# Kernel tuning notes

Hardware: AMD Instinct MI355X
Metric: run time of the kernel (lower is better)

Reference implementation:

```python
import math
import jax, jax.numpy as jnp
import numpy as np

BSZ, N_HEADS, N_KV_HEADS, SEQLEN, HEAD_DIM = 1, 32, 8, 2048, 128
DIM = N_HEADS * HEAD_DIM  # 4096
N_REP = N_HEADS // N_KV_HEADS  # 4
NEG = -1e9


def setup_inputs() -> dict:
    key = jax.random.key(0)
    kq, kk, kv = jax.random.split(key, 3)
    q = jax.random.normal(kq, (BSZ, N_HEADS, SEQLEN, HEAD_DIM), dtype=jnp.float32)
    k = jax.random.normal(kk, (BSZ, N_KV_HEADS, SEQLEN, HEAD_DIM), dtype=jnp.float32)
    v = jax.random.normal(kv, (BSZ, N_KV_HEADS, SEQLEN, HEAD_DIM), dtype=jnp.float32)
    # additive causal mask: 0 on/below diagonal, large negative above
    causal = jnp.tril(jnp.ones((SEQLEN, SEQLEN), dtype=bool))
    mask = jnp.where(causal, 0.0, NEG).astype(jnp.float32)
    input_pos = jnp.zeros((1,), dtype=jnp.int64)
    return {"input_pos": input_pos, "q": q, "k": k, "v": v,
            "bsz": BSZ, "seqlen": SEQLEN, "mask": mask}


def reference(input_pos, q, k, v, bsz, seqlen, mask):
    # repeat_kv: (b, n_kv, s, d) -> (b, n_kv*n_rep, s, d), repeat_interleave on head dim
    k = jnp.repeat(k, N_REP, axis=1)
    v = jnp.repeat(v, N_REP, axis=1)
    scale = 1.0 / math.sqrt(q.shape[-1])
    # (b, h, s, s)
    attn = jnp.einsum("bhqd,bhkd->bhqk", q, k) * scale + mask
    attn = jax.nn.softmax(attn, axis=-1)
    y = jnp.einsum("bhqk,bhkd->bhqd", attn, v)  # (b, h, s, d)
    return y.transpose(0, 2, 1, 3).reshape(bsz, seqlen, DIM)
```

## Files before the change

### kernel.cpp

```cpp
#include <hip/hip_runtime.h>
#include <hip/hip_bf16.h>

#define SEQ 2048
#define HD 128
#define NH 32
#define NKV 8
#define ODIM 4096
#define QB 64
#define KVB 64
#define SCALE 0.08838834764831845f
#define SCALE_L2E 0.12752767f
#define NEGBIG -1e9f
#define NEGBIG_L2 -1.4426950e9f
#define THR_L2 11.54f

typedef __attribute__((ext_vector_type(8))) short bf16x8;
typedef __attribute__((ext_vector_type(4))) float f32x4;

__device__ __forceinline__ unsigned short f2bf(float x) {
  union { __hip_bfloat16 b; unsigned short u; } c;
  c.b = __float2bfloat16(x);
  return c.u;
}

__device__ __forceinline__ unsigned pack2bf(float lo, float hi) {
  union { __hip_bfloat162 h; unsigned u; } c;
  c.h = __float22bfloat162_rn(float2{lo, hi});
  return c.u;
}

__device__ __forceinline__ void gload_lds16(const unsigned char* g, unsigned char* l) {
  __builtin_amdgcn_global_load_lds(
      (const __attribute__((address_space(1))) void*)g,
      (__attribute__((address_space(3))) void*)l, 16, 0, 0);
}

#define KWORK (NKV * SEQ * 16)
#define VWORK (NKV * (SEQ / 2) * 16)
__global__ __launch_bounds__(256) void sdpa_prepass(
    const float* __restrict__ k, const float* __restrict__ v,
    unsigned char* __restrict__ ws) {
  unsigned char* kimg = ws;
  unsigned char* vimg = ws + (NKV * 32 * 16384);
  int idx = (int)blockIdx.x * 256 + (int)threadIdx.x;
  if (idx < KWORK) {
    int hkv = idx >> 15;
    int rem = idx & 32767;
    int rg = rem >> 4;
    int c8 = (rem & 15) << 3;
    const float* src = k + ((size_t)hkv * SEQ + rg) * HD + c8;
    float4 a = *(const float4*)(src);
    float4 b = *(const float4*)(src + 4);
    union { unsigned short hh[8]; uint4 u4; } pk;
    pk.hh[0]=f2bf(a.x); pk.hh[1]=f2bf(a.y); pk.hh[2]=f2bf(a.z); pk.hh[3]=f2bf(a.w);
    pk.hh[4]=f2bf(b.x); pk.hh[5]=f2bf(b.y); pk.hh[6]=f2bf(b.z); pk.hh[7]=f2bf(b.w);
    int t = rg >> 6, r = rg & 63;
    size_t base = ((size_t)(hkv * 32 + t)) << 14;
    *(uint4*)(kimg + base + (r << 8) + ((c8 << 1) ^ ((r & 7) << 4))) = pk.u4;
  } else {
    int u = idx - KWORK;
    if (u >= VWORK) return;
    int hkv = u >> 14;
    int rem = u & 16383;
    int pr = rem >> 4;
    int d0 = (rem & 15) << 3;
    int rg = pr << 1;
    const float* s0 = v + ((size_t)hkv * SEQ + rg) * HD + d0;
    const float* s1 = s0 + HD;
    float4 a0 = *(const float4*)(s0);
    float4 b0 = *(const float4*)(s0 + 4);
    float4 a1 = *(const float4*)(s1);
    float4 b1 = *(const float4*)(s1 + 4);
    float lo[8] = {a0.x,a0.y,a0.z,a0.w,b0.x,b0.y,b0.z,b0.w};
    float hi[8] = {a1.x,a1.y,a1.z,a1.w,b1.x,b1.y,b1.z,b1.w};
    int t = rg >> 6, rr = rg & 63;
    size_t base = ((size_t)(hkv * 32 + t)) << 14;
    int rb = rr << 1;
    #pragma unroll
    for (int j = 0; j < 8; ++j) {
      int d = d0 + j;
      *(unsigned*)(vimg + base + (d << 7) + (rb ^ ((d & 7) << 4))) =
          pack2bf(lo[j], hi[j]);
    }
  }
}

__global__ __launch_bounds__(512, 4) void sdpa_flash_kernel(
    const float* __restrict__ q, const unsigned char* __restrict__ kimg,
    const unsigned char* __restrict__ vimg, float* __restrict__ out) {
  __shared__ __align__(16) unsigned char smem[65536];
  const int tid = threadIdx.x;
  const int w = tid >> 6;
  const int l = tid & 63;
  const int lm = l & 15;
  const int lg = l >> 4;

  const int p = (int)blockIdx.x;
  const int qtA = p;
  const int qtB = 31 - p;
  const int myqt = (w < 4) ? qtA : qtB;
  const int h = (int)blockIdx.y;
  const int hkv = h >> 2;
  const int qbase = myqt * QB + 16 * (w & 3);
  const int myrow = qbase + lm;

  bf16x8 qa[4];
  {
    const float* qr = q + ((size_t)(h * SEQ + myrow)) * HD + 8 * lg;
    #pragma unroll
    for (int c = 0; c < 4; ++c) {
      float4 a = *(const float4*)(qr + 32 * c);
      float4 b = *(const float4*)(qr + 32 * c + 4);
      union { unsigned short hh[8]; bf16x8 vv; } pk;
      pk.hh[0] = f2bf(a.x * SCALE_L2E); pk.hh[1] = f2bf(a.y * SCALE_L2E);
      pk.hh[2] = f2bf(a.z * SCALE_L2E); pk.hh[3] = f2bf(a.w * SCALE_L2E);
      pk.hh[4] = f2bf(b.x * SCALE_L2E); pk.hh[5] = f2bf(b.y * SCALE_L2E);
      pk.hh[6] = f2bf(b.z * SCALE_L2E); pk.hh[7] = f2bf(b.w * SCALE_L2E);
      qa[c] = pk.vv;
    }
  }

  f32x4 o[8];
  #pragma unroll
  for (int i = 0; i < 8; ++i) o[i] = (f32x4){0.f, 0.f, 0.f, 0.f};
  float mrow = -1e30f;
  float lrow = 0.f;

  const int ntiles = qtB + 1;
  const unsigned char* kt0 = kimg + (((size_t)(hkv * 32)) << 14);
  const unsigned char* vt0 = vimg + (((size_t)(hkv * 32)) << 14);
  const int woff = w << 10;

#define STAGE(tt, bufbase) {                                                 \
    const unsigned char* ks_ = kt0 + (((size_t)(tt)) << 14);                 \
    const unsigned char* vs_ = vt0 + (((size_t)(tt)) << 14);                 \
    unsigned char* Kb_ = (bufbase);                                          \
    unsigned char* Vb_ = (bufbase) + 16384;                                  \
    gload_lds16(ks_ + woff + (l << 4), Kb_ + woff);                          \
    gload_lds16(ks_ + 8192 + woff + (l << 4), Kb_ + 8192 + woff);            \
    gload_lds16(vs_ + woff + (l << 4), Vb_ + woff);                          \
    gload_lds16(vs_ + 8192 + woff + (l << 4), Vb_ + 8192 + woff);            \
  }

  STAGE(0, smem);
  __syncthreads();
  int cur = 0;

  for (int t = 0; t < ntiles; ++t) {
    const int kv0 = t * KVB;
    if (t + 1 < ntiles) STAGE(t + 1, smem + ((cur ^ 1) << 15));

    unsigned char* Klds = smem + (cur << 15);
    unsigned char* Vlds = Klds + 16384;

    if (t <= myqt) {
      f32x4 s[4];
      #pragma unroll
      for (int nt = 0; nt < 4; ++nt) s[nt] = (f32x4){0.f, 0.f, 0.f, 0.f};
      __builtin_amdgcn_s_setprio(1);
      #pragma unroll
      for (int nt = 0; nt < 4; ++nt) {
        int r = (nt << 4) + lm;
        #pragma unroll
        for (int kc = 0; kc < 4; ++kc) {
          int byte = (r << 8) + (((kc << 6) + (lg << 4)) ^ ((r & 7) << 4));
          bf16x8 kb = *(const bf16x8*)(Klds + byte);
          s[nt] = __builtin_amdgcn_mfma_f32_16x16x32_bf16(kb, qa[kc], s[nt], 0, 0, 0);
        }
      }
      __builtin_amdgcn_s_setprio(0);

      if (kv0 + KVB - 1 > qbase) {
        #pragma unroll
        for (int nt = 0; nt < 4; ++nt) {
          #pragma unroll
          for (int i = 0; i < 4; ++i) {
            int col = kv0 + (nt << 4) + (lg << 2) + i;
            s[nt][i] += (col > myrow) ? NEGBIG_L2 : 0.f;
          }
        }
      }

      float tm = -1e30f;
      #pragma unroll
      for (int nt = 0; nt < 4; ++nt)
        #pragma unroll
        for (int i = 0; i < 4; ++i) tm = fmaxf(tm, s[nt][i]);
      tm = fmaxf(tm, __shfl_xor(tm, 16));
      tm = fmaxf(tm, __shfl_xor(tm, 32));
      if (!__all(tm <= mrow + THR_L2)) {
        float mn = fmaxf(mrow, tm);
        float fac = __builtin_amdgcn_exp2f(mrow - mn);
        mrow = mn;
        lrow *= fac;
        #pragma unroll
        for (int nt2 = 0; nt2 < 8; ++nt2) {
          #pragma unroll
          for (int i = 0; i < 4; ++i) o[nt2][i] *= fac;
        }
      }
      float rs = 0.f;
      #pragma unroll
      for (int nt = 0; nt < 4; ++nt) {
        #pragma unroll
        for (int i = 0; i < 4; ++i) {
          float pv = __builtin_amdgcn_exp2f(s[nt][i] - mrow);
          s[nt][i] = pv;
          rs += pv;
        }
      }
      rs += __shfl_xor(rs, 16);
      rs += __shfl_xor(rs, 32);
      lrow += rs;

      unsigned pk0[4], pk1[4];
      #pragma unroll
      for (int nt = 0; nt < 4; ++nt) {
        pk0[nt] = pack2bf(s[nt][0], s[nt][1]);
        pk1[nt] = pack2bf(s[nt][2], s[nt][3]);
      }
      const int srcA = lm + ((lg & 1) << 5);
      const int srcB = srcA + 16;
      const bool lo2 = (lg < 2);
      bf16x8 pb[2];
      #pragma unroll
      for (int kc = 0; kc < 2; ++kc) {
        int a0 = __shfl((int)pk0[2*kc], srcA), b0 = __shfl((int)pk0[2*kc+1], srcA);
        int a1 = __shfl((int)pk1[2*kc], srcA), b1 = __shfl((int)pk1[2*kc+1], srcA);
        int a2 = __shfl((int)pk0[2*kc], srcB), b2 = __shfl((int)pk0[2*kc+1], srcB);
        int a3 = __shfl((int)pk1[2*kc], srcB), b3 = __shfl((int)pk1[2*kc+1], srcB);
        union { int uu[4]; bf16x8 v; } pw;
        pw.uu[0] = lo2 ? a0 : b0;
        pw.uu[1] = lo2 ? a1 : b1;
        pw.uu[2] = lo2 ? a2 : b2;
        pw.uu[3] = lo2 ? a3 : b3;
        pb[kc] = pw.v;
      }

      __builtin_amdgcn_s_setprio(1);
      #pragma unroll
      for (int nt2 = 0; nt2 < 8; ++nt2) {
        int dr = (nt2 << 4) + lm;
        #pragma unroll
        for (int kc = 0; kc < 2; ++kc) {
          int byte = (dr << 7) + (((kc << 6) + (lg << 4)) ^ ((dr & 7) << 4));
          bf16x8 vb = *(const bf16x8*)(Vlds + byte);
          o[nt2] = __builtin_amdgcn_mfma_f32_16x16x32_bf16(vb, pb[kc], o[nt2], 0, 0, 0);
        }
      }
      __builtin_amdgcn_s_setprio(0);
    }

    __syncthreads();
    cur ^= 1;
  }

  float inv = 1.f / lrow;
  float* orow = out + (size_t)myrow * ODIM + h * HD + (lg << 2);
  #pragma unroll
  for (int nt2 = 0; nt2 < 8; ++nt2) {
    float4 st = {o[nt2][0] * inv, o[nt2][1] * inv, o[nt2][2] * inv, o[nt2][3] * inv};
    *(float4*)(orow + (nt2 << 4)) = st;
  }
#undef STAGE
}

__global__ __launch_bounds__(512, 4) void sdpa_flash_fb(
    const float* __restrict__ q, const float* __restrict__ k,
    const float* __restrict__ v, float* __restrict__ out) {
  __shared__ __align__(16) unsigned char smem[65536];
  const int tid = threadIdx.x;
  const int w = tid >> 6;
  const int l = tid & 63;
  const int lm = l & 15;
  const int lg = l >> 4;
  const int p = (int)blockIdx.x;
  const int qtA = p;
  const int qtB = 31 - p;
  const int myqt = (w < 4) ? qtA : qtB;
  const int h = (int)blockIdx.y;
  const int hkv = h >> 2;
  const int qbase = myqt * QB + 16 * (w & 3);
  const int myrow = qbase + lm;
  bf16x8 qa[4];
  {
    const float* qr = q + ((size_t)(h * SEQ + myrow)) * HD + 8 * lg;
    #pragma unroll
    for (int c = 0; c < 4; ++c) {
      float4 a = *(const float4*)(qr + 32 * c);
      float4 b = *(const float4*)(qr + 32 * c + 4);
      union { unsigned short hh[8]; bf16x8 vv; } pk;
      pk.hh[0] = f2bf(a.x * SCALE); pk.hh[1] = f2bf(a.y * SCALE);
      pk.hh[2] = f2bf(a.z * SCALE); pk.hh[3] = f2bf(a.w * SCALE);
      pk.hh[4] = f2bf(b.x * SCALE); pk.hh[5] = f2bf(b.y * SCALE);
      pk.hh[6] = f2bf(b.z * SCALE); pk.hh[7] = f2bf(b.w * SCALE);
      qa[c] = pk.vv;
    }
  }
  f32x4 o[8];
  #pragma unroll
  for (int i = 0; i < 8; ++i) o[i] = (f32x4){0.f, 0.f, 0.f, 0.f};
  float mrow = -1e30f;
  float lrow = 0.f;
  const int ntiles = qtB + 1;
  const float* kg0 = k + (size_t)hkv * SEQ * HD;
  const float* vg0 = v + (size_t)hkv * SEQ * HD;
  const int k_r0 = tid >> 4;
  const int k_c8 = (tid & 15) << 3;
  const int v_rr = (tid & 31) << 1;
  const int v_d0 = (tid >> 5) << 3;
  float4 ka0, kb0, ka1, kb1, va0, vb0, va1, vb1;
#define LOADT(tt) {                                                          \
    const float* kg_ = kg0 + (size_t)((tt) * KVB) * HD + k_r0 * HD + k_c8;   \
    ka0 = *(const float4*)(kg_);                                             \
    kb0 = *(const float4*)(kg_ + 4);                                         \
    ka1 = *(const float4*)(kg_ + 32 * HD);                                   \
    kb1 = *(const float4*)(kg_ + 32 * HD + 4);                               \
    const float* vg_ = vg0 + (size_t)((tt) * KVB) * HD + v_rr * HD + v_d0;   \
    va0 = *(const float4*)(vg_);                                             \
    vb0 = *(const float4*)(vg_ + 4);                                         \
    va1 = *(const float4*)(vg_ + HD);                                        \
    vb1 = *(const float4*)(vg_ + HD + 4);                                    \
  }
#define WRITELDS(bufbase) {                                                  \
    unsigned char* Kb_ = (bufbase);                                          \
    unsigned char* Vb_ = (bufbase) + 16384;                                  \
    {                                                                        \
      union { unsigned short hh[8]; uint4 u4; } pk_;                         \
      pk_.hh[0]=f2bf(ka0.x); pk_.hh[1]=f2bf(ka0.y);                          \
      pk_.hh[2]=f2bf(ka0.z); pk_.hh[3]=f2bf(ka0.w);                          \
      pk_.hh[4]=f2bf(kb0.x); pk_.hh[5]=f2bf(kb0.y);                          \
      pk_.hh[6]=f2bf(kb0.z); pk_.hh[7]=f2bf(kb0.w);                          \
      int byte_ = (k_r0 << 8) + ((k_c8 << 1) ^ ((k_r0 & 7) << 4));           \
      *(uint4*)(Kb_ + byte_) = pk_.u4;                                       \
    }                                                                        \
    {                                                                        \
      int r1_ = k_r0 + 32;                                                   \
      union { unsigned short hh[8]; uint4 u4; } pk_;                         \
      pk_.hh[0]=f2bf(ka1.x); pk_.hh[1]=f2bf(ka1.y);                          \
      pk_.hh[2]=f2bf(ka1.z); pk_.hh[3]=f2bf(ka1.w);                          \
      pk_.hh[4]=f2bf(kb1.x); pk_.hh[5]=f2bf(kb1.y);                          \
      pk_.hh[6]=f2bf(kb1.z); pk_.hh[7]=f2bf(kb1.w);                          \
      int byte_ = (r1_ << 8) + ((k_c8 << 1) ^ ((r1_ & 7) << 4));             \
      *(uint4*)(Kb_ + byte_) = pk_.u4;                                       \
    }                                                                        \
    {                                                                        \
      unsigned w0_ = pack2bf(va0.x, va1.x), w1_ = pack2bf(va0.y, va1.y);     \
      unsigned w2_ = pack2bf(va0.z, va1.z), w3_ = pack2bf(va0.w, va1.w);     \
      unsigned w4_ = pack2bf(vb0.x, vb1.x), w5_ = pack2bf(vb0.y, vb1.y);     \
      unsigned w6_ = pack2bf(vb0.z, vb1.z), w7_ = pack2bf(vb0.w, vb1.w);     \
      int rb_ = v_rr << 1;                                                   \
      int d_;                                                                \
      d_ = v_d0;     *(unsigned*)(Vb_ + (d_ << 7) + (rb_ ^ ((d_ & 7) << 4))) = w0_; \
      d_ = v_d0 + 1; *(unsigned*)(Vb_ + (d_ << 7) + (rb_ ^ ((d_ & 7) << 4))) = w1_; \
      d_ = v_d0 + 2; *(unsigned*)(Vb_ + (d_ << 7) + (rb_ ^ ((d_ & 7) << 4))) = w2_; \
      d_ = v_d0 + 3; *(unsigned*)(Vb_ + (d_ << 7) + (rb_ ^ ((d_ & 7) << 4))) = w3_; \
      d_ = v_d0 + 4; *(unsigned*)(Vb_ + (d_ << 7) + (rb_ ^ ((d_ & 7) << 4))) = w4_; \
      d_ = v_d0 + 5; *(unsigned*)(Vb_ + (d_ << 7) + (rb_ ^ ((d_ & 7) << 4))) = w5_; \
      d_ = v_d0 + 6; *(unsigned*)(Vb_ + (d_ << 7) + (rb_ ^ ((d_ & 7) << 4))) = w6_; \
      d_ = v_d0 + 7; *(unsigned*)(Vb_ + (d_ << 7) + (rb_ ^ ((d_ & 7) << 4))) = w7_; \
    }                                                                        \
  }
  LOADT(0);
  WRITELDS(smem);
  __syncthreads();
  int cur = 0;
  for (int t = 0; t < ntiles; ++t) {
    const int kv0 = t * KVB;
    const bool have_next = (t + 1 < ntiles);
    if (have_next) LOADT(t + 1);
    unsigned char* Klds = smem + (cur << 15);
    unsigned char* Vlds = Klds + 16384;
    if (t <= myqt) {
      f32x4 s[4];
      #pragma unroll
      for (int nt = 0; nt < 4; ++nt) s[nt] = (f32x4){0.f, 0.f, 0.f, 0.f};
      #pragma unroll
      for (int nt = 0; nt < 4; ++nt) {
        int r = (nt << 4) + lm;
        #pragma unroll
        for (int kc = 0; kc < 4; ++kc) {
          int byte = (r << 8) + (((kc << 6) + (lg << 4)) ^ ((r & 7) << 4));
          bf16x8 kb = *(const bf16x8*)(Klds + byte);
          s[nt] = __builtin_amdgcn_mfma_f32_16x16x32_bf16(kb, qa[kc], s[nt], 0, 0, 0);
        }
      }
      if (kv0 + KVB - 1 > qbase) {
        #pragma unroll
        for (int nt = 0; nt < 4; ++nt) {
          #pragma unroll
          for (int i = 0; i < 4; ++i) {
            int col = kv0 + (nt << 4) + (lg << 2) + i;
            s[nt][i] += (col > myrow) ? NEGBIG : 0.f;
          }
        }
      }
      float tm = -1e30f;
      #pragma unroll
      for (int nt = 0; nt < 4; ++nt)
        #pragma unroll
        for (int i = 0; i < 4; ++i) tm = fmaxf(tm, s[nt][i]);
      tm = fmaxf(tm, __shfl_xor(tm, 16));
      tm = fmaxf(tm, __shfl_xor(tm, 32));
      float mn = fmaxf(mrow, tm);
      float fac = __expf(mrow - mn);
      mrow = mn;
      float rs = 0.f;
      #pragma unroll
      for (int nt = 0; nt < 4; ++nt) {
        #pragma unroll
        for (int i = 0; i < 4; ++i) {
          float pv = __expf(s[nt][i] - mn);
          s[nt][i] = pv;
          rs += pv;
        }
      }
      rs += __shfl_xor(rs, 16);
      rs += __shfl_xor(rs, 32);
      lrow = lrow * fac + rs;
      #pragma unroll
      for (int nt2 = 0; nt2 < 8; ++nt2) {
        #pragma unroll
        for (int i = 0; i < 4; ++i) o[nt2][i] *= fac;
      }
      unsigned pk0[4], pk1[4];
      #pragma unroll
      for (int nt = 0; nt < 4; ++nt) {
        pk0[nt] = pack2bf(s[nt][0], s[nt][1]);
        pk1[nt] = pack2bf(s[nt][2], s[nt][3]);
      }
      const int srcA = lm + ((lg & 1) << 5);
      const int srcB = srcA + 16;
      const bool lo2 = (lg < 2);
      bf16x8 pb[2];
      #pragma unroll
      for (int kc = 0; kc < 2; ++kc) {
        int a0 = __shfl((int)pk0[2*kc], srcA), b0 = __shfl((int)pk0[2*kc+1], srcA);
        int a1 = __shfl((int)pk1[2*kc], srcA), b1 = __shfl((int)pk1[2*kc+1], srcA);
        int a2 = __shfl((int)pk0[2*kc], srcB), b2 = __shfl((int)pk0[2*kc+1], srcB);
        int a3 = __shfl((int)pk1[2*kc], srcB), b3 = __shfl((int)pk1[2*kc+1], srcB);
        union { int uu[4]; bf16x8 v; } pw;
        pw.uu[0] = lo2 ? a0 : b0;
        pw.uu[1] = lo2 ? a1 : b1;
        pw.uu[2] = lo2 ? a2 : b2;
        pw.uu[3] = lo2 ? a3 : b3;
        pb[kc] = pw.v;
      }
      #pragma unroll
      for (int nt2 = 0; nt2 < 8; ++nt2) {
        int dr = (nt2 << 4) + lm;
        #pragma unroll
        for (int kc = 0; kc < 2; ++kc) {
          int byte = (dr << 7) + (((kc << 6) + (lg << 4)) ^ ((dr & 7) << 4));
          bf16x8 vb = *(const bf16x8*)(Vlds + byte);
          o[nt2] = __builtin_amdgcn_mfma_f32_16x16x32_bf16(vb, pb[kc], o[nt2], 0, 0, 0);
        }
      }
    }
    if (have_next) {
      WRITELDS(smem + ((cur ^ 1) << 15));
    }
    __syncthreads();
    cur ^= 1;
  }
  float inv = 1.f / lrow;
  float* orow = out + (size_t)myrow * ODIM + h * HD + (lg << 2);
  #pragma unroll
  for (int nt2 = 0; nt2 < 8; ++nt2) {
    float4 st = {o[nt2][0] * inv, o[nt2][1] * inv, o[nt2][2] * inv, o[nt2][3] * inv};
    *(float4*)(orow + (nt2 << 4)) = st;
  }
#undef LOADT
#undef WRITELDS
}

extern "C" void kernel_launch(void* const* d_in, const int* in_sizes, int n_in,
                              void* d_out, int out_size, void* d_ws, size_t ws_size,
                              hipStream_t stream) {
  const float* q = (const float*)d_in[1];
  const float* k = (const float*)d_in[2];
  const float* v = (const float*)d_in[3];
  float* out = (float*)d_out;
  dim3 grid(SEQ / QB / 2, NH);
  const size_t need = (size_t)(NKV * 32 * 16384) * 2;
  if (ws_size >= need && d_ws != nullptr) {
    unsigned char* ws = (unsigned char*)d_ws;
    int total = KWORK + VWORK;
    sdpa_prepass<<<(total + 255) / 256, 256, 0, stream>>>(k, v, ws);
    sdpa_flash_kernel<<<grid, 512, 0, stream>>>(
        q, ws, ws + (NKV * 32 * 16384), out);
  } else {
    sdpa_flash_fb<<<grid, 512, 0, stream>>>(q, k, v, out);
  }
}
```

Measured before the change: 85.98 us.

## Shrink KV tile to 32 rows and use one q-tile per 256-thread block

Halves the KV tile from 64 to 32 rows and re-lays out the prepacked V image to match 32-row tiles. Drops the paired-q-tile scheme: each 256-thread block now handles a single 64-row query tile, launched in descending tile order, with per-wave causal tile limits that skip fully masked half-tiles. The aim is to cut wasted masked compute at the diagonal and let more, smaller blocks share each CU. In exchange it runs twice as many KV-loop iterations, each with a barrier, and load balancing now depends on dispatch order rather than explicit pairing.

```diff
diff --git a/kernel.cpp b/kernel.cpp
--- a/kernel.cpp
+++ b/kernel.cpp
@@ -8,6 +8,7 @@
 #define ODIM 4096
 #define QB 64
 #define KVB 64
+#define KVT 32
 #define SCALE 0.08838834764831845f
 #define SCALE_L2E 0.12752767f
 #define NEGBIG -1e9f
@@ -41,7 +42,7 @@
     const float* __restrict__ k, const float* __restrict__ v,
     unsigned char* __restrict__ ws) {
   unsigned char* kimg = ws;
-  unsigned char* vimg = ws + (NKV * 32 * 16384);
+  unsigned char* vimg = ws + ((size_t)NKV << 19);
   int idx = (int)blockIdx.x * 256 + (int)threadIdx.x;
   if (idx < KWORK) {
     int hkv = idx >> 15;
@@ -54,9 +55,8 @@
     union { unsigned short hh[8]; uint4 u4; } pk;
     pk.hh[0]=f2bf(a.x); pk.hh[1]=f2bf(a.y); pk.hh[2]=f2bf(a.z); pk.hh[3]=f2bf(a.w);
     pk.hh[4]=f2bf(b.x); pk.hh[5]=f2bf(b.y); pk.hh[6]=f2bf(b.z); pk.hh[7]=f2bf(b.w);
-    int t = rg >> 6, r = rg & 63;
-    size_t base = ((size_t)(hkv * 32 + t)) << 14;
-    *(uint4*)(kimg + base + (r << 8) + ((c8 << 1) ^ ((r & 7) << 4))) = pk.u4;
+    size_t base = ((size_t)hkv << 19) + ((size_t)rg << 8);
+    *(uint4*)(kimg + base + ((c8 << 1) ^ ((rg & 7) << 4))) = pk.u4;
   } else {
     int u = idx - KWORK;
     if (u >= VWORK) return;
@@ -73,35 +73,32 @@
     float4 b1 = *(const float4*)(s1 + 4);
     float lo[8] = {a0.x,a0.y,a0.z,a0.w,b0.x,b0.y,b0.z,b0.w};
     float hi[8] = {a1.x,a1.y,a1.z,a1.w,b1.x,b1.y,b1.z,b1.w};
-    int t = rg >> 6, rr = rg & 63;
-    size_t base = ((size_t)(hkv * 32 + t)) << 14;
-    int rb = rr << 1;
+    int t32 = rg >> 5;
+    size_t base = ((size_t)(hkv * 64 + t32)) << 13;
+    int rb = (rg & 31) << 1;
     #pragma unroll
     for (int j = 0; j < 8; ++j) {
       int d = d0 + j;
-      *(unsigned*)(vimg + base + (d << 7) + (rb ^ ((d & 7) << 4))) =
+      *(unsigned*)(vimg + base + (d << 6) + (rb ^ ((d & 3) << 4))) =
           pack2bf(lo[j], hi[j]);
     }
   }
 }
 
-__global__ __launch_bounds__(512, 4) void sdpa_flash_kernel(
+__global__ __launch_bounds__(256, 4) void sdpa_flash_kernel(
     const float* __restrict__ q, const unsigned char* __restrict__ kimg,
     const unsigned char* __restrict__ vimg, float* __restrict__ out) {
-  __shared__ __align__(16) unsigned char smem[65536];
+  __shared__ __align__(16) unsigned char smem[32768];
   const int tid = threadIdx.x;
   const int w = tid >> 6;
   const int l = tid & 63;
   const int lm = l & 15;
   const int lg = l >> 4;
 
-  const int p = (int)blockIdx.x;
-  const int qtA = p;
-  const int qtB = 31 - p;
-  const int myqt = (w < 4) ? qtA : qtB;
+  const int qt = 31 - (int)blockIdx.x;
   const int h = (int)blockIdx.y;
   const int hkv = h >> 2;
-  const int qbase = myqt * QB + 16 * (w & 3);
+  const int qbase = qt * QB + 16 * w;
   const int myrow = qbase + lm;
 
   bf16x8 qa[4];
@@ -126,20 +123,21 @@
   float mrow = -1e30f;
   float lrow = 0.f;
 
-  const int ntiles = qtB + 1;
-  const unsigned char* kt0 = kimg + (((size_t)(hkv * 32)) << 14);
-  const unsigned char* vt0 = vimg + (((size_t)(hkv * 32)) << 14);
-  const int woff = w << 10;
+  const int ntiles = 2 * qt + 2;
+  const int tlim = 2 * qt + (w >> 1);
+  const unsigned char* kt0 = kimg + ((size_t)hkv << 19);
+  const unsigned char* vt0 = vimg + ((size_t)hkv << 19);
+  const int woff = w << 11;
 
 #define STAGE(tt, bufbase) {                                                 \
-    const unsigned char* ks_ = kt0 + (((size_t)(tt)) << 14);                 \
-    const unsigned char* vs_ = vt0 + (((size_t)(tt)) << 14);                 \
+    const unsigned char* ks_ = kt0 + (((size_t)(tt)) << 13);                 \
+    const unsigned char* vs_ = vt0 + (((size_t)(tt)) << 13);                 \
     unsigned char* Kb_ = (bufbase);                                          \
-    unsigned char* Vb_ = (bufbase) + 16384;                                  \
+    unsigned char* Vb_ = (bufbase) + 8192;                                   \
     gload_lds16(ks_ + woff + (l << 4), Kb_ + woff);                          \
-    gload_lds16(ks_ + 8192 + woff + (l << 4), Kb_ + 8192 + woff);            \
+    gload_lds16(ks_ + woff + 1024 + (l << 4), Kb_ + woff + 1024);            \
     gload_lds16(vs_ + woff + (l << 4), Vb_ + woff);                          \
-    gload_lds16(vs_ + 8192 + woff + (l << 4), Vb_ + 8192 + woff);            \
+    gload_lds16(vs_ + woff + 1024 + (l << 4), Vb_ + woff + 1024);            \
   }
 
   STAGE(0, smem);
@@ -147,19 +145,19 @@
   int cur = 0;
 
   for (int t = 0; t < ntiles; ++t) {
-    const int kv0 = t * KVB;
-    if (t + 1 < ntiles) STAGE(t + 1, smem + ((cur ^ 1) << 15));
-
-    unsigned char* Klds = smem + (cur << 15);
-    unsigned char* Vlds = Klds + 16384;
-
-    if (t <= myqt) {
-      f32x4 s[4];
-      #pragma unroll
-      for (int nt = 0; nt < 4; ++nt) s[nt] = (f32x4){0.f, 0.f, 0.f, 0.f};
+    const int kv0 = t * KVT;
+    if (t + 1 < ntiles) STAGE(t + 1, smem + ((cur ^ 1) << 14));
+
+    unsigned char* Klds = smem + (cur << 14);
+    unsigned char* Vlds = Klds + 8192;
+
+    if (t <= tlim) {
+      f32x4 s[2];
+      #pragma unroll
+      for (int nt = 0; nt < 2; ++nt) s[nt] = (f32x4){0.f, 0.f, 0.f, 0.f};
       __builtin_amdgcn_s_setprio(1);
       #pragma unroll
-      for (int nt = 0; nt < 4; ++nt) {
+      for (int nt = 0; nt < 2; ++nt) {
         int r = (nt << 4) + lm;
         #pragma unroll
         for (int kc = 0; kc < 4; ++kc) {
@@ -170,9 +168,9 @@
       }
       __builtin_amdgcn_s_setprio(0);
 
-      if (kv0 + KVB - 1 > qbase) {
-        #pragma unroll
-        for (int nt = 0; nt < 4; ++nt) {
+      if (kv0 + KVT - 1 > qbase) {
+        #pragma unroll
+        for (int nt = 0; nt < 2; ++nt) {
           #pragma unroll
           for (int i = 0; i < 4; ++i) {
             int col = kv0 + (nt << 4) + (lg << 2) + i;
@@ -183,7 +181,7 @@
 
       float tm = -1e30f;
       #pragma unroll
-      for (int nt = 0; nt < 4; ++nt)
+      for (int nt = 0; nt < 2; ++nt)
         #pragma unroll
         for (int i = 0; i < 4; ++i) tm = fmaxf(tm, s[nt][i]);
       tm = fmaxf(tm, __shfl_xor(tm, 16));
@@ -201,7 +199,7 @@
       }
       float rs = 0.f;
       #pragma unroll
-      for (int nt = 0; nt < 4; ++nt) {
+      for (int nt = 0; nt < 2; ++nt) {
         #pragma unroll
         for (int i = 0; i < 4; ++i) {
           float pv = __builtin_amdgcn_exp2f(s[nt][i] - mrow);
@@ -213,40 +211,36 @@
       rs += __shfl_xor(rs, 32);
       lrow += rs;
 
-      unsigned pk0[4], pk1[4];
-      #pragma unroll
-      for (int nt = 0; nt < 4; ++nt) {
+      unsigned pk0[2], pk1[2];
+      #pragma unroll
+      for (int nt = 0; nt < 2; ++nt) {
         pk0[nt] = pack2bf(s[nt][0], s[nt][1]);
         pk1[nt] = pack2bf(s[nt][2], s[nt][3]);
       }
       const int srcA = lm + ((lg & 1) << 5);
       const int srcB = srcA + 16;
       const bool lo2 = (lg < 2);
-      bf16x8 pb[2];
-      #pragma unroll
-      for (int kc = 0; kc < 2; ++kc) {
-        int a0 = __shfl((int)pk0[2*kc], srcA), b0 = __shfl((int)pk0[2*kc+1], srcA);
-        int a1 = __shfl((int)pk1[2*kc], srcA), b1 = __shfl((int)pk1[2*kc+1], srcA);
-        int a2 = __shfl((int)pk0[2*kc], srcB), b2 = __shfl((int)pk0[2*kc+1], srcB);
-        int a3 = __shfl((int)pk1[2*kc], srcB), b3 = __shfl((int)pk1[2*kc+1], srcB);
+      bf16x8 pb;
+      {
+        int a0 = __shfl((int)pk0[0], srcA), b0 = __shfl((int)pk0[1], srcA);
+        int a1 = __shfl((int)pk1[0], srcA), b1 = __shfl((int)pk1[1], srcA);
+        int a2 = __shfl((int)pk0[0], srcB), b2 = __shfl((int)pk0[1], srcB);
+        int a3 = __shfl((int)pk1[0], srcB), b3 = __shfl((int)pk1[1], srcB);
         union { int uu[4]; bf16x8 v; } pw;
         pw.uu[0] = lo2 ? a0 : b0;
         pw.uu[1] = lo2 ? a1 : b1;
         pw.uu[2] = lo2 ? a2 : b2;
         pw.uu[3] = lo2 ? a3 : b3;
-        pb[kc] = pw.v;
+        pb = pw.v;
       }
 
       __builtin_amdgcn_s_setprio(1);
       #pragma unroll
       for (int nt2 = 0; nt2 < 8; ++nt2) {
         int dr = (nt2 << 4) + lm;
-        #pragma unroll
-        for (int kc = 0; kc < 2; ++kc) {
-          int byte = (dr << 7) + (((kc << 6) + (lg << 4)) ^ ((dr & 7) << 4));
-          bf16x8 vb = *(const bf16x8*)(Vlds + byte);
-          o[nt2] = __builtin_amdgcn_mfma_f32_16x16x32_bf16(vb, pb[kc], o[nt2], 0, 0, 0);
-        }
+        int byte = (dr << 6) + ((lg << 4) ^ ((dr & 3) << 4));
+        bf16x8 vb = *(const bf16x8*)(Vlds + byte);
+        o[nt2] = __builtin_amdgcn_mfma_f32_16x16x32_bf16(vb, pb, o[nt2], 0, 0, 0);
       }
       __builtin_amdgcn_s_setprio(0);
     }
@@ -481,15 +475,16 @@
   const float* k = (const float*)d_in[2];
   const float* v = (const float*)d_in[3];
   float* out = (float*)d_out;
-  dim3 grid(SEQ / QB / 2, NH);
-  const size_t need = (size_t)(NKV * 32 * 16384) * 2;
+  const size_t need = ((size_t)NKV << 19) * 2;
   if (ws_size >= need && d_ws != nullptr) {
     unsigned char* ws = (unsigned char*)d_ws;
     int total = KWORK + VWORK;
     sdpa_prepass<<<(total + 255) / 256, 256, 0, stream>>>(k, v, ws);
-    sdpa_flash_kernel<<<grid, 512, 0, stream>>>(
-        q, ws, ws + (NKV * 32 * 16384), out);
+    dim3 grid(SEQ / QB, NH);
+    sdpa_flash_kernel<<<grid, 256, 0, stream>>>(
+        q, ws, ws + ((size_t)NKV << 19), out);
   } else {
-    sdpa_flash_fb<<<grid, 512, 0, stream>>>(q, k, v, out);
-  }
-}
+    dim3 gridf(SEQ / QB / 2, NH);
+    sdpa_flash_fb<<<gridf, 512, 0, stream>>>(q, k, v, out);
+  }
+}
```

New measurement: 137.0 us. +59.4%, slower.

## Software-pipeline QK^T of next tile with softmax and PV of previous tile

Applied to the files above, without the earlier changes.

Restructures the flash-attention loop so each iteration computes QK^T scores for tile t while doing softmax and PV for tile t-1, carrying scores in registers. V moves to a 3-slot LDS ring (LDS grows to 80KB), with K double-buffered separately, and an epilogue drains the last tile. The aim is to overlap MFMA work with the exp/shuffle softmax chain. In exchange it raises register and LDS pressure, which can lower occupancy, and the final-tile handling for waves with smaller myqt relies on subtle slot bookkeeping.

```diff
diff --git a/kernel.cpp b/kernel.cpp
--- a/kernel.cpp
+++ b/kernel.cpp
@@ -88,7 +88,8 @@
 __global__ __launch_bounds__(512, 4) void sdpa_flash_kernel(
     const float* __restrict__ q, const unsigned char* __restrict__ kimg,
     const unsigned char* __restrict__ vimg, float* __restrict__ out) {
-  __shared__ __align__(16) unsigned char smem[65536];
+  __shared__ __align__(16) unsigned char smem[81920];
+  unsigned char* Vring = smem + 32768;
   const int tid = threadIdx.x;
   const int w = tid >> 6;
   const int l = tid & 63;
@@ -131,61 +132,75 @@
   const unsigned char* vt0 = vimg + (((size_t)(hkv * 32)) << 14);
   const int woff = w << 10;
 
-#define STAGE(tt, bufbase) {                                                 \
+#define STAGE(tt, Kb, Vb) {                                                  \
     const unsigned char* ks_ = kt0 + (((size_t)(tt)) << 14);                 \
     const unsigned char* vs_ = vt0 + (((size_t)(tt)) << 14);                 \
-    unsigned char* Kb_ = (bufbase);                                          \
-    unsigned char* Vb_ = (bufbase) + 16384;                                  \
-    gload_lds16(ks_ + woff + (l << 4), Kb_ + woff);                          \
-    gload_lds16(ks_ + 8192 + woff + (l << 4), Kb_ + 8192 + woff);            \
-    gload_lds16(vs_ + woff + (l << 4), Vb_ + woff);                          \
-    gload_lds16(vs_ + 8192 + woff + (l << 4), Vb_ + 8192 + woff);            \
-  }
-
-  STAGE(0, smem);
+    gload_lds16(ks_ + woff + (l << 4), (Kb) + woff);                         \
+    gload_lds16(ks_ + 8192 + woff + (l << 4), (Kb) + 8192 + woff);           \
+    gload_lds16(vs_ + woff + (l << 4), (Vb) + woff);                         \
+    gload_lds16(vs_ + 8192 + woff + (l << 4), (Vb) + 8192 + woff);           \
+  }
+
+  STAGE(0, smem, Vring);
   __syncthreads();
-  int cur = 0;
+
+  f32x4 sp0, sp1, sp2, sp3;
+  int slot_cur = 0;
+  int slot_prev = 0;
 
   for (int t = 0; t < ntiles; ++t) {
     const int kv0 = t * KVB;
-    if (t + 1 < ntiles) STAGE(t + 1, smem + ((cur ^ 1) << 15));
-
-    unsigned char* Klds = smem + (cur << 15);
-    unsigned char* Vlds = Klds + 16384;
-
-    if (t <= myqt) {
-      f32x4 s[4];
-      #pragma unroll
-      for (int nt = 0; nt < 4; ++nt) s[nt] = (f32x4){0.f, 0.f, 0.f, 0.f};
+    int slot_next = slot_cur + 1; if (slot_next == 3) slot_next = 0;
+    if (t + 1 < ntiles)
+      STAGE(t + 1, smem + ((t + 1) & 1) * 16384, Vring + slot_next * 16384);
+
+    unsigned char* Klds = smem + (t & 1) * 16384;
+
+    f32x4 sc0, sc1, sc2, sc3;
+    const bool doQK = (t <= myqt);
+    if (doQK) {
+      sc0 = (f32x4){0.f,0.f,0.f,0.f}; sc1 = (f32x4){0.f,0.f,0.f,0.f};
+      sc2 = (f32x4){0.f,0.f,0.f,0.f}; sc3 = (f32x4){0.f,0.f,0.f,0.f};
       __builtin_amdgcn_s_setprio(1);
       #pragma unroll
-      for (int nt = 0; nt < 4; ++nt) {
-        int r = (nt << 4) + lm;
-        #pragma unroll
-        for (int kc = 0; kc < 4; ++kc) {
-          int byte = (r << 8) + (((kc << 6) + (lg << 4)) ^ ((r & 7) << 4));
-          bf16x8 kb = *(const bf16x8*)(Klds + byte);
-          s[nt] = __builtin_amdgcn_mfma_f32_16x16x32_bf16(kb, qa[kc], s[nt], 0, 0, 0);
+      for (int kc = 0; kc < 4; ++kc) {
+        int r0 = lm;
+        int byte0 = (r0 << 8) + (((kc << 6) + (lg << 4)) ^ ((r0 & 7) << 4));
+        bf16x8 kb0 = *(const bf16x8*)(Klds + byte0);
+        sc0 = __builtin_amdgcn_mfma_f32_16x16x32_bf16(kb0, qa[kc], sc0, 0, 0, 0);
+        int r1 = 16 + lm;
+        int byte1 = (r1 << 8) + (((kc << 6) + (lg << 4)) ^ ((r1 & 7) << 4));
+        bf16x8 kb1 = *(const bf16x8*)(Klds + byte1);
+        sc1 = __builtin_amdgcn_mfma_f32_16x16x32_bf16(kb1, qa[kc], sc1, 0, 0, 0);
+        int r2 = 32 + lm;
+        int byte2 = (r2 << 8) + (((kc << 6) + (lg << 4)) ^ ((r2 & 7) << 4));
+        bf16x8 kb2 = *(const bf16x8*)(Klds + byte2);
+        sc2 = __builtin_amdgcn_mfma_f32_16x16x32_bf16(kb2, qa[kc], sc2, 0, 0, 0);
+        int r3 = 48 + lm;
+        int byte3 = (r3 << 8) + (((kc << 6) + (lg << 4)) ^ ((r3 & 7) << 4));
+        bf16x8 kb3 = *(const bf16x8*)(Klds + byte3);
+        sc3 = __builtin_amdgcn_mfma_f32_16x16x32_bf16(kb3, qa[kc], sc3, 0, 0, 0);
+      }
+      __builtin_amdgcn_s_setprio(0);
+      if (kv0 + KVB - 1 > qbase) {
+        #pragma unroll
+        for (int i = 0; i < 4; ++i) {
+          int colb = kv0 + (lg << 2) + i;
+          sc0[i] += (colb > myrow) ? NEGBIG_L2 : 0.f;
+          sc1[i] += (colb + 16 > myrow) ? NEGBIG_L2 : 0.f;
+          sc2[i] += (colb + 32 > myrow) ? NEGBIG_L2 : 0.f;
+          sc3[i] += (colb + 48 > myrow) ? NEGBIG_L2 : 0.f;
         }
       }
-      __builtin_amdgcn_s_setprio(0);
-
-      if (kv0 + KVB - 1 > qbase) {
-        #pragma unroll
-        for (int nt = 0; nt < 4; ++nt) {
-          #pragma unroll
-          for (int i = 0; i < 4; ++i) {
-            int col = kv0 + (nt << 4) + (lg << 2) + i;
-            s[nt][i] += (col > myrow) ? NEGBIG_L2 : 0.f;
-          }
-        }
-      }
-
+    }
+
+    if (t >= 1 && t - 1 <= myqt) {
+      unsigned char* Vlds = Vring + slot_prev * 16384;
       float tm = -1e30f;
       #pragma unroll
-      for (int nt = 0; nt < 4; ++nt)
-        #pragma unroll
-        for (int i = 0; i < 4; ++i) tm = fmaxf(tm, s[nt][i]);
+      for (int i = 0; i < 4; ++i) {
+        tm = fmaxf(tm, fmaxf(fmaxf(sp0[i], sp1[i]), fmaxf(sp2[i], sp3[i])));
+      }
       tm = fmaxf(tm, __shfl_xor(tm, 16));
       tm = fmaxf(tm, __shfl_xor(tm, 32));
       if (!__all(tm <= mrow + THR_L2)) {
@@ -194,47 +209,53 @@
         mrow = mn;
         lrow *= fac;
         #pragma unroll
-        for (int nt2 = 0; nt2 < 8; ++nt2) {
+        for (int nt2 = 0; nt2 < 8; ++nt2)
           #pragma unroll
           for (int i = 0; i < 4; ++i) o[nt2][i] *= fac;
-        }
       }
       float rs = 0.f;
       #pragma unroll
-      for (int nt = 0; nt < 4; ++nt) {
-        #pragma unroll
-        for (int i = 0; i < 4; ++i) {
-          float pv = __builtin_amdgcn_exp2f(s[nt][i] - mrow);
-          s[nt][i] = pv;
-          rs += pv;
-        }
+      for (int i = 0; i < 4; ++i) {
+        sp0[i] = __builtin_amdgcn_exp2f(sp0[i] - mrow); rs += sp0[i];
+        sp1[i] = __builtin_amdgcn_exp2f(sp1[i] - mrow); rs += sp1[i];
+        sp2[i] = __builtin_amdgcn_exp2f(sp2[i] - mrow); rs += sp2[i];
+        sp3[i] = __builtin_amdgcn_exp2f(sp3[i] - mrow); rs += sp3[i];
       }
       rs += __shfl_xor(rs, 16);
       rs += __shfl_xor(rs, 32);
       lrow += rs;
 
-      unsigned pk0[4], pk1[4];
-      #pragma unroll
-      for (int nt = 0; nt < 4; ++nt) {
-        pk0[nt] = pack2bf(s[nt][0], s[nt][1]);
-        pk1[nt] = pack2bf(s[nt][2], s[nt][3]);
-      }
+      unsigned pa0 = pack2bf(sp0[0], sp0[1]), pa1 = pack2bf(sp0[2], sp0[3]);
+      unsigned pb0 = pack2bf(sp1[0], sp1[1]), pb1 = pack2bf(sp1[2], sp1[3]);
+      unsigned pc0 = pack2bf(sp2[0], sp2[1]), pc1 = pack2bf(sp2[2], sp2[3]);
+      unsigned pd0 = pack2bf(sp3[0], sp3[1]), pd1 = pack2bf(sp3[2], sp3[3]);
       const int srcA = lm + ((lg & 1) << 5);
       const int srcB = srcA + 16;
       const bool lo2 = (lg < 2);
       bf16x8 pb[2];
-      #pragma unroll
-      for (int kc = 0; kc < 2; ++kc) {
-        int a0 = __shfl((int)pk0[2*kc], srcA), b0 = __shfl((int)pk0[2*kc+1], srcA);
-        int a1 = __shfl((int)pk1[2*kc], srcA), b1 = __shfl((int)pk1[2*kc+1], srcA);
-        int a2 = __shfl((int)pk0[2*kc], srcB), b2 = __shfl((int)pk0[2*kc+1], srcB);
-        int a3 = __shfl((int)pk1[2*kc], srcB), b3 = __shfl((int)pk1[2*kc+1], srcB);
+      {
+        int a0 = __shfl((int)pa0, srcA), b0 = __shfl((int)pb0, srcA);
+        int a1 = __shfl((int)pa1, srcA), b1 = __shfl((int)pb1, srcA);
+        int a2 = __shfl((int)pa0, srcB), b2 = __shfl((int)pb0, srcB);
+        int a3 = __shfl((int)pa1, srcB), b3 = __shfl((int)pb1, srcB);
         union { int uu[4]; bf16x8 v; } pw;
         pw.uu[0] = lo2 ? a0 : b0;
         pw.uu[1] = lo2 ? a1 : b1;
         pw.uu[2] = lo2 ? a2 : b2;
         pw.uu[3] = lo2 ? a3 : b3;
-        pb[kc] = pw.v;
+        pb[0] = pw.v;
+      }
+      {
+        int a0 = __shfl((int)pc0, srcA), b0 = __shfl((int)pd0, srcA);
+        int a1 = __shfl((int)pc1, srcA), b1 = __shfl((int)pd1, srcA);
+        int a2 = __shfl((int)pc0, srcB), b2 = __shfl((int)pd0, srcB);
+        int a3 = __shfl((int)pc1, srcB), b3 = __shfl((int)pd1, srcB);
+        union { int uu[4]; bf16x8 v; } pw;
+        pw.uu[0] = lo2 ? a0 : b0;
+        pw.uu[1] = lo2 ? a1 : b1;
+        pw.uu[2] = lo2 ? a2 : b2;
+        pw.uu[3] = lo2 ? a3 : b3;
+        pb[1] = pw.v;
       }
 
       __builtin_amdgcn_s_setprio(1);
@@ -251,8 +272,85 @@
       __builtin_amdgcn_s_setprio(0);
     }
 
+    if (doQK) { sp0 = sc0; sp1 = sc1; sp2 = sc2; sp3 = sc3; }
+
     __syncthreads();
-    cur ^= 1;
+    slot_prev = slot_cur;
+    slot_cur = slot_next;
+  }
+
+  if (myqt == ntiles - 1) {
+    unsigned char* Vlds = Vring + slot_prev * 16384;
+    float tm = -1e30f;
+    #pragma unroll
+    for (int i = 0; i < 4; ++i)
+      tm = fmaxf(tm, fmaxf(fmaxf(sp0[i], sp1[i]), fmaxf(sp2[i], sp3[i])));
+    tm = fmaxf(tm, __shfl_xor(tm, 16));
+    tm = fmaxf(tm, __shfl_xor(tm, 32));
+    if (!__all(tm <= mrow + THR_L2)) {
+      float mn = fmaxf(mrow, tm);
+      float fac = __builtin_amdgcn_exp2f(mrow - mn);
+      mrow = mn;
+      lrow *= fac;
+      #pragma unroll
+      for (int nt2 = 0; nt2 < 8; ++nt2)
+        #pragma unroll
+        for (int i = 0; i < 4; ++i) o[nt2][i] *= fac;
+    }
+    float rs = 0.f;
+    #pragma unroll
+    for (int i = 0; i < 4; ++i) {
+      sp0[i] = __builtin_amdgcn_exp2f(sp0[i] - mrow); rs += sp0[i];
+      sp1[i] = __builtin_amdgcn_exp2f(sp1[i] - mrow); rs += sp1[i];
+      sp2[i] = __builtin_amdgcn_exp2f(sp2[i] - mrow); rs += sp2[i];
+      sp3[i] = __builtin_amdgcn_exp2f(sp3[i] - mrow); rs += sp3[i];
+    }
+    rs += __shfl_xor(rs, 16);
+    rs += __shfl_xor(rs, 32);
+    lrow += rs;
+
+    unsigned pa0 = pack2bf(sp0[0], sp0[1]), pa1 = pack2bf(sp0[2], sp0[3]);
+    unsigned pb0 = pack2bf(sp1[0], sp1[1]), pb1 = pack2bf(sp1[2], sp1[3]);
+    unsigned pc0 = pack2bf(sp2[0], sp2[1]), pc1 = pack2bf(sp2[2], sp2[3]);
+    unsigned pd0 = pack2bf(sp3[0], sp3[1]), pd1 = pack2bf(sp3[2], sp3[3]);
+    const int srcA = lm + ((lg & 1) << 5);
+    const int srcB = srcA + 16;
+    const bool lo2 = (lg < 2);
+    bf16x8 pb[2];
+    {
+      int a0 = __shfl((int)pa0, srcA), b0 = __shfl((int)pb0, srcA);
+      int a1 = __shfl((int)pa1, srcA), b1 = __shfl((int)pb1, srcA);
+      int a2 = __shfl((int)pa0, srcB), b2 = __shfl((int)pb0, srcB);
+      int a3 = __shfl((int)pa1, srcB), b3 = __shfl((int)pb1, srcB);
+      union { int uu[4]; bf16x8 v; } pw;
+      pw.uu[0] = lo2 ? a0 : b0;
+      pw.uu[1] = lo2 ? a1 : b1;
+      pw.uu[2] = lo2 ? a2 : b2;
+      pw.uu[3] = lo2 ? a3 : b3;
+      pb[0] = pw.v;
+    }
+    {
+      int a0 = __shfl((int)pc0, srcA), b0 = __shfl((int)pd0, srcA);
+      int a1 = __shfl((int)pc1, srcA), b1 = __shfl((int)pd1, srcA);
+      int a2 = __shfl((int)pc0, srcB), b2 = __shfl((int)pd0, srcB);
+      int a3 = __shfl((int)pc1, srcB), b3 = __shfl((int)pd1, srcB);
+      union { int uu[4]; bf16x8 v; } pw;
+      pw.uu[0] = lo2 ? a0 : b0;
+      pw.uu[1] = lo2 ? a1 : b1;
+      pw.uu[2] = lo2 ? a2 : b2;
+      pw.uu[3] = lo2 ? a3 : b3;
+      pb[1] = pw.v;
+    }
+    #pragma unroll
+    for (int nt2 = 0; nt2 < 8; ++nt2) {
+      int dr = (nt2 << 4) + lm;
+      #pragma unroll
+      for (int kc = 0; kc < 2; ++kc) {
+        int byte = (dr << 7) + (((kc << 6) + (lg << 4)) ^ ((dr & 7) << 4));
+        bf16x8 vb = *(const bf16x8*)(Vlds + byte);
+        o[nt2] = __builtin_amdgcn_mfma_f32_16x16x32_bf16(vb, pb[kc], o[nt2], 0, 0, 0);
+      }
+    }
   }
 
   float inv = 1.f / lrow;
```

Result: slower. 89.27 us (+3.8%).

## Replace double-buffered K/V LDS with three rotating 16KB buffers

Applied to the files above, without the earlier changes.

Cuts shared memory per block from 64KB to 48KB by rotating three 16KB buffers: the next K tile is prefetched into a free buffer while the current K is used for QK^T. After a mid-iteration barrier, the next V tile is loaded into the just-freed K buffer. Launch bounds are raised to allow more resident blocks per CU. The cost is an extra __syncthreads per tile and less prefetch distance for V, and the higher occupancy target may force register spills.

```diff
diff --git a/kernel.cpp b/kernel.cpp
--- a/kernel.cpp
+++ b/kernel.cpp
@@ -85,10 +85,10 @@
   }
 }
 
-__global__ __launch_bounds__(512, 4) void sdpa_flash_kernel(
+__global__ __launch_bounds__(512, 6) void sdpa_flash_kernel(
     const float* __restrict__ q, const unsigned char* __restrict__ kimg,
     const unsigned char* __restrict__ vimg, float* __restrict__ out) {
-  __shared__ __align__(16) unsigned char smem[65536];
+  __shared__ __align__(16) unsigned char smem[49152];
   const int tid = threadIdx.x;
   const int w = tid >> 6;
   const int l = tid & 63;
@@ -131,30 +131,33 @@
   const unsigned char* vt0 = vimg + (((size_t)(hkv * 32)) << 14);
   const int woff = w << 10;
 
-#define STAGE(tt, bufbase) {                                                 \
+#define STAGE_K(tt, Kb) {                                                    \
     const unsigned char* ks_ = kt0 + (((size_t)(tt)) << 14);                 \
+    gload_lds16(ks_ + woff + (l << 4), (Kb) + woff);                         \
+    gload_lds16(ks_ + 8192 + woff + (l << 4), (Kb) + 8192 + woff);           \
+  }
+#define STAGE_V(tt, Vb) {                                                    \
     const unsigned char* vs_ = vt0 + (((size_t)(tt)) << 14);                 \
-    unsigned char* Kb_ = (bufbase);                                          \
-    unsigned char* Vb_ = (bufbase) + 16384;                                  \
-    gload_lds16(ks_ + woff + (l << 4), Kb_ + woff);                          \
-    gload_lds16(ks_ + 8192 + woff + (l << 4), Kb_ + 8192 + woff);            \
-    gload_lds16(vs_ + woff + (l << 4), Vb_ + woff);                          \
-    gload_lds16(vs_ + 8192 + woff + (l << 4), Vb_ + 8192 + woff);            \
-  }
-
-  STAGE(0, smem);
+    gload_lds16(vs_ + woff + (l << 4), (Vb) + woff);                         \
+    gload_lds16(vs_ + 8192 + woff + (l << 4), (Vb) + 8192 + woff);           \
+  }
+
+  unsigned char* sA = smem;
+  unsigned char* sB = smem + 16384;
+  unsigned char* sC = smem + 32768;
+
+  STAGE_K(0, sA);
+  STAGE_V(0, sB);
   __syncthreads();
-  int cur = 0;
 
   for (int t = 0; t < ntiles; ++t) {
     const int kv0 = t * KVB;
-    if (t + 1 < ntiles) STAGE(t + 1, smem + ((cur ^ 1) << 15));
-
-    unsigned char* Klds = smem + (cur << 15);
-    unsigned char* Vlds = Klds + 16384;
-
-    if (t <= myqt) {
-      f32x4 s[4];
+    const bool have_next = (t + 1 < ntiles);
+    if (have_next) STAGE_K(t + 1, sC);
+
+    const bool act = (t <= myqt);
+    f32x4 s[4];
+    if (act) {
       #pragma unroll
       for (int nt = 0; nt < 4; ++nt) s[nt] = (f32x4){0.f, 0.f, 0.f, 0.f};
       __builtin_amdgcn_s_setprio(1);
@@ -164,7 +167,7 @@
         #pragma unroll
         for (int kc = 0; kc < 4; ++kc) {
           int byte = (r << 8) + (((kc << 6) + (lg << 4)) ^ ((r & 7) << 4));
-          bf16x8 kb = *(const bf16x8*)(Klds + byte);
+          bf16x8 kb = *(const bf16x8*)(sA + byte);
           s[nt] = __builtin_amdgcn_mfma_f32_16x16x32_bf16(kb, qa[kc], s[nt], 0, 0, 0);
         }
       }
@@ -180,7 +183,12 @@
           }
         }
       }
-
+    }
+
+    __syncthreads();
+    if (have_next) STAGE_V(t + 1, sA);
+
+    if (act) {
       float tm = -1e30f;
       #pragma unroll
       for (int nt = 0; nt < 4; ++nt)
@@ -244,7 +252,7 @@
         #pragma unroll
         for (int kc = 0; kc < 2; ++kc) {
           int byte = (dr << 7) + (((kc << 6) + (lg << 4)) ^ ((dr & 7) << 4));
-          bf16x8 vb = *(const bf16x8*)(Vlds + byte);
+          bf16x8 vb = *(const bf16x8*)(sB + byte);
           o[nt2] = __builtin_amdgcn_mfma_f32_16x16x32_bf16(vb, pb[kc], o[nt2], 0, 0, 0);
         }
       }
@@ -252,7 +260,10 @@
     }
 
     __syncthreads();
-    cur ^= 1;
+    unsigned char* nA = sC;
+    unsigned char* nB = sA;
+    unsigned char* nC = sB;
+    sA = nA; sB = nB; sC = nC;
   }
 
   float inv = 1.f / lrow;
@@ -262,7 +273,8 @@
     float4 st = {o[nt2][0] * inv, o[nt2][1] * inv, o[nt2][2] * inv, o[nt2][3] * inv};
     *(float4*)(orow + (nt2 << 4)) = st;
   }
-#undef STAGE
+#undef STAGE_K
+#undef STAGE_V
 }
 
 __global__ __launch_bounds__(512, 4) void sdpa_flash_fb(
```

Result: slower. 134.0 us (+55.8%).
